# Kernel tuning notes

Measured on AMD Instinct MI355X. Metric: run time of the kernel, lower is better.

Reference implementation:

```python
import jax, jax.numpy as jnp
import numpy as np

KERNEL_SIZE = 13
SIGMA_MIN, SIGMA_MAX = 0.4, 10.0
BETA, THRESHOLD = 0.95, 1.0


@jax.custom_vjp
def spike(x):
    # Heaviside forward, snntorch ATan surrogate backward (alpha=2)
    return (x > 0).astype(x.dtype)

def _spike_fwd(x):
    return spike(x), x

def _spike_bwd(x, g):
    return (g / (1.0 + (jnp.pi * x) ** 2),)

spike.defvjp(_spike_fwd, _spike_bwd)


def setup_inputs() -> dict:
    key = jax.random.key(0)
    k1, k2 = jax.random.split(key)
    B, C, T = 32, 224, 2048
    inp = jax.random.normal(k1, (B, 1, C, T), dtype=jnp.float32)
    linear_w = jax.random.normal(k2, (1, C), dtype=jnp.float32) * (1.0 / np.sqrt(C))
    return {"inp": inp, "linear_w": linear_w}


def _forward(inp, linear_w):
    x = inp[:, 0]  # [B, C, T]
    B, C, T = x.shape
    sigma_mean = 0.5 * (SIGMA_MIN + SIGMA_MAX)
    # adaptive sigma per (batch, time): Linear over channel axis, no bias
    w = sigma_mean + jnp.einsum('bct,c->bt', x, linear_w[0]) * (SIGMA_MAX - SIGMA_MIN)
    w = jnp.clip(w, SIGMA_MIN, SIGMA_MAX)  # [B, T]

    half = KERNEL_SIZE // 2
    r = jnp.linspace(-half, half, KERNEL_SIZE)
    r_all = jnp.linspace(-half * 10, half * 10, KERNEL_SIZE * 10)
    sig = w[..., None]  # [B, T, 1]
    kern = jnp.exp(-0.5 * (r / sig) ** 2)                       # [B, T, K]
    norm = jnp.exp(-0.5 * (r_all / sig) ** 2).sum(-1, keepdims=True)
    kern = kern / norm                                          # normalized over fine grid

    # adaptive gaussian smoothing along the CHANNEL axis (per timestep kernel)
    xt = jnp.transpose(x, (0, 2, 1))                            # [B, T, C]
    padded = jnp.pad(xt, ((0, 0), (0, 0), (half, half)))        # zero pad channels
    x_mean = sum(padded[:, :, k:k + C] * kern[:, :, k:k + 1]
                 for k in range(KERNEL_SIZE))                   # [B, T, C]
    x_mean = jnp.transpose(x_mean, (0, 2, 1))                   # [B, C, T]

    I = x - jax.nn.relu(x - x_mean)                             # soft min(x, x_mean)

    # Leaky-integrate-and-fire over time (snntorch Leaky, reset-by-subtract)
    def step(mem, I_t):
        reset = jax.lax.stop_gradient((mem > THRESHOLD).astype(I_t.dtype))
        mem = BETA * mem + I_t - reset * THRESHOLD
        spk = spike(mem - THRESHOLD)
        return mem, spk

    I_seq = jnp.transpose(I, (2, 0, 1))                         # [T, B, C]
    _, spk = jax.lax.scan(step, jnp.zeros((B, C), I.dtype), I_seq)
    spk = jnp.transpose(spk, (1, 2, 0))                         # [B, C, T]
    return spk[:, None]                                         # [B, 1, C, T]


def reference(inp, linear_w):
    return _forward(inp, linear_w)
```

## Files before the change

kernel.cpp:

```cpp
#include <hip/hip_runtime.h>
#include <math.h>

#define BB 32
#define CCH 224
#define TTT 2048
#define TPB 64
#define NT  (TTT/TPB)
#define CG  28
#define NCG (CCH/CG)
#define ROWS 40
#define XROW 68
#define IROW 29

__global__ __launch_bounds__(256) void kw(
    const float* __restrict__ x, const float* __restrict__ lw,
    double* __restrict__ kernG)
{
    __shared__ double sp[4][64];
    const int b  = blockIdx.y;
    const int tl = threadIdx.x & 63;
    const int q  = threadIdx.x >> 6;
    const int t  = blockIdx.x * 64 + tl;

    const float* xb  = x + (((size_t)(b * CCH + 56 * q)) << 11) + t;
    const float* lwq = lw + 56 * q;

    double p = 0.0;
    #pragma unroll 8
    for (int i = 0; i < 56; ++i)
        p += (double)xb[(size_t)i << 11] * (double)lwq[i];
    sp[q][tl] = p;
    __syncthreads();

    if (threadIdx.x < 64) {
        double acc = (sp[0][tl] + sp[1][tl]) + (sp[2][tl] + sp[3][tl]);

        double w = 5.2 + acc * 9.6;
        w = fmin(fmax(w, 0.4), 10.0);
        double iw2 = 1.0 / (w * w);

        const double s = 120.0 / 129.0;
        double G  = exp(-0.125 * s * s * iw2);
        double G2 = G * G, G4 = G2 * G2, G8 = G4 * G4;
        double term = G, cmul = G8, norm = G;
        for (int u = 1; u <= 64; ++u) { term *= cmul; cmul *= G8; norm += term; }
        norm *= 2.0;

        double P = exp(-0.5 * iw2), P2 = P * P;
        double a = 1.0, bm = P, inv = 1.0 / norm;
        double* kr = kernG + (size_t)(b * TTT + t) * 7;
        kr[0] = inv;
        #pragma unroll
        for (int d = 1; d <= 6; ++d) {
            a *= bm; bm *= P2;
            kr[d] = a * inv;
        }
    }
}

__global__ __launch_bounds__(320) void kf(
    const float* __restrict__ x, const double* __restrict__ kernG,
    float* __restrict__ out)
{
    __shared__ __align__(16) float xs[2][ROWS][XROW];
    __shared__ double kd[2][TPB][7];
    __shared__ double Is[2][TPB][IROW];
    __shared__ unsigned long long bitsb[2][CG];

    const int b   = blockIdx.y;
    const int cgi = blockIdx.x;
    const int c0  = cgi * CG;
    const int tid = threadIdx.x;
    const int ctid = tid - 64;

    const float*  xbase = x + (((size_t)(b * CCH)) << 11);
    const double* kbase = kernG + (size_t)(b * TTT) * 7;
    float* obase = out + (((size_t)(b * CCH + c0)) << 11);

    double mem = 0.0;
    bool   r   = false;

    if (tid >= 64) {
        #pragma unroll
        for (int i2 = 0; i2 < 3; ++i2) {
            int e = ctid + i2 * 256;
            if (e < ROWS * 16) {
                int rr = e >> 4, q = e & 15;
                int cr = c0 - 6 + rr;
                float4 v = make_float4(0.f, 0.f, 0.f, 0.f);
                if (cr >= 0 && cr < CCH)
                    v = *(const float4*)(xbase + ((size_t)cr << 11) + 4 * q);
                *(float4*)&xs[0][rr][4 * q] = v;
            }
        }
        if (ctid < TPB) {
            const double* kp = kbase + (size_t)ctid * 7;
            #pragma unroll
            for (int i2 = 0; i2 < 7; ++i2) kd[0][ctid][i2] = kp[i2];
        }
    }
    __syncthreads();

    for (int k = 0; k <= NT + 1; ++k) {
        if (tid >= 64) {
            const int buf = k & 1, nbuf = (k + 1) & 1;
            float4 rv[3]; double kv[7];
            const bool st = (k + 1 <= NT - 1);
            if (st) {
                const int gt0 = (k + 1) * TPB;
                #pragma unroll
                for (int i2 = 0; i2 < 3; ++i2) {
                    int e = ctid + i2 * 256;
                    if (e < ROWS * 16) {
                        int rr = e >> 4, q = e & 15;
                        int cr = c0 - 6 + rr;
                        rv[i2] = make_float4(0.f, 0.f, 0.f, 0.f);
                        if (cr >= 0 && cr < CCH)
                            rv[i2] = *(const float4*)(xbase + ((size_t)cr << 11) + gt0 + 4 * q);
                    }
                }
                if (ctid < TPB) {
                    const double* kp = kbase + (size_t)(gt0 + ctid) * 7;
                    #pragma unroll
                    for (int i2 = 0; i2 < 7; ++i2) kv[i2] = kp[i2];
                }
            }
            if (k <= NT - 1) {
                const int t  = ctid & 63;
                const int ch = ctid >> 6;
                const int cb = 7 * ch;
                double kk7[7];
                #pragma unroll
                for (int i2 = 0; i2 < 7; ++i2) kk7[i2] = kd[buf][t][i2];
                float xv[13];
                #pragma unroll
                for (int i2 = 0; i2 < 13; ++i2) xv[i2] = xs[buf][cb + i2][t];
                #pragma unroll
                for (int c = 0; c < 7; ++c) {
                    double acc = 0.0;
                    #pragma unroll
                    for (int kk2 = 0; kk2 < 13; ++kk2) {
                        int d = kk2 < 6 ? 6 - kk2 : kk2 - 6;
                        acc = fma((double)xv[(c + kk2) % 13], kk7[d], acc);
                    }
                    double xvv = (double)xv[(c + 6) % 13];
                    double dd  = xvv - acc;
                    Is[buf][t][cb + c] = xvv - (dd > 0.0 ? dd : 0.0);
                    if (c < 6) xv[c % 13] = xs[buf][cb + c + 13][t];
                }
            }
            if (k >= 2) {
                const int j = k - 2, jb = j & 1;
                const int t0o = j * TPB;
                #pragma unroll
                for (int i2 = 0; i2 < 2; ++i2) {
                    int e = ctid + i2 * 256;
                    if (e < CG * 16) {
                        int c = e >> 4, q = e & 15;
                        unsigned long long bits = bitsb[jb][c] >> (4 * q);
                        float4 v;
                        v.x = (bits & 1ull) ? 1.0f : 0.0f;
                        v.y = (bits & 2ull) ? 1.0f : 0.0f;
                        v.z = (bits & 4ull) ? 1.0f : 0.0f;
                        v.w = (bits & 8ull) ? 1.0f : 0.0f;
                        *(float4*)(obase + ((size_t)c << 11) + t0o + 4 * q) = v;
                    }
                }
            }
            if (st) {
                #pragma unroll
                for (int i2 = 0; i2 < 3; ++i2) {
                    int e = ctid + i2 * 256;
                    if (e < ROWS * 16) {
                        int rr = e >> 4, q = e & 15;
                        *(float4*)&xs[nbuf][rr][4 * q] = rv[i2];
                    }
                }
                if (ctid < TPB) {
                    #pragma unroll
                    for (int i2 = 0; i2 < 7; ++i2) kd[nbuf][ctid][i2] = kv[i2];
                }
            }
        } else {
            if (k >= 1 && k <= NT) {
                const int p = (k - 1) & 1;
                const int c = tid;
                if (c < CG) {
                    unsigned long long bits = 0ull;
                    double va[8], vb[8];
                    #pragma unroll
                    for (int j2 = 0; j2 < 8; ++j2) va[j2] = Is[p][j2][c];
                    #pragma unroll
                    for (int g = 0; g < 64; g += 16) {
                        #pragma unroll
                        for (int j2 = 0; j2 < 8; ++j2) vb[j2] = Is[p][g + 8 + j2][c];
                        #pragma unroll
                        for (int j2 = 0; j2 < 8; ++j2) {
                            double a2 = va[j2];
                            double cm = a2 - 1.0;
                            double m1 = fma(0.95, mem, a2);
                            double m2 = fma(0.95, mem, cm);
                            mem = r ? m2 : m1;
                            r = mem > 1.0;
                            bits |= (unsigned long long)(r ? 1 : 0) << (g + j2);
                        }
                        if (g + 16 < 64) {
                            #pragma unroll
                            for (int j2 = 0; j2 < 8; ++j2) va[j2] = Is[p][g + 16 + j2][c];
                        }
                        #pragma unroll
                        for (int j2 = 0; j2 < 8; ++j2) {
                            double a2 = vb[j2];
                            double cm = a2 - 1.0;
                            double m1 = fma(0.95, mem, a2);
                            double m2 = fma(0.95, mem, cm);
                            mem = r ? m2 : m1;
                            r = mem > 1.0;
                            bits |= (unsigned long long)(r ? 1 : 0) << (g + 8 + j2);
                        }
                    }
                    bitsb[p][c] = bits;
                }
            }
        }
        __syncthreads();
    }
}

extern "C" void kernel_launch(void* const* d_in, const int* in_sizes, int n_in,
                              void* d_out, int out_size, void* d_ws, size_t ws_size,
                              hipStream_t stream)
{
    const float* x  = (const float*)d_in[0];
    const float* lw = (const float*)d_in[1];
    float* out = (float*)d_out;

    double* kernG = (double*)d_ws;

    kw<<<dim3(TTT / 64, BB), 256, 0, stream>>>(x, lw, kernG);
    kf<<<dim3(NCG, BB), 320, 0, stream>>>(x, kernG, out);
}
```

Baseline: 152.1 us.

## Deepen prefetch to two tiles ahead, raise scan wave priority, use LDS-only barrier

Global loads for the x and kernel-weight tiles are now issued two iterations ahead and held in registers across the barrier, with the LDS store of the previous prefetch done at the start of each iteration. This hides global-memory latency behind a full iteration of compute. The serial LIF scan wave gets raised instruction priority via s_setprio, since it sits on the critical path. __syncthreads is replaced by a barrier that waits only on lgkmcnt, so outstanding global loads do not stall the barrier. The cost is more live registers across iterations, and correctness now depends on global loads not being needed before the barrier.

```diff
diff --git a/kernel.cpp b/kernel.cpp
--- a/kernel.cpp
+++ b/kernel.cpp
@@ -12,6 +12,12 @@
 #define XROW 68
 #define IROW 29
 
+__device__ __forceinline__ void bar_lds() {
+    asm volatile("s_waitcnt lgkmcnt(0)" ::: "memory");
+    __builtin_amdgcn_s_barrier();
+    asm volatile("" ::: "memory");
+}
+
 __global__ __launch_bounds__(256) void kw(
     const float* __restrict__ x, const float* __restrict__ lw,
     double* __restrict__ kernG)
@@ -79,6 +85,8 @@
 
     double mem = 0.0;
     bool   r   = false;
+
+    float4 rv[3]; double kv[7];
 
     if (tid >= 64) {
         #pragma unroll
@@ -98,16 +106,47 @@
             #pragma unroll
             for (int i2 = 0; i2 < 7; ++i2) kd[0][ctid][i2] = kp[i2];
         }
+        {
+            const int gt0 = TPB;
+            #pragma unroll
+            for (int i2 = 0; i2 < 3; ++i2) {
+                int e = ctid + i2 * 256;
+                if (e < ROWS * 16) {
+                    int rr = e >> 4, q = e & 15;
+                    int cr = c0 - 6 + rr;
+                    rv[i2] = make_float4(0.f, 0.f, 0.f, 0.f);
+                    if (cr >= 0 && cr < CCH)
+                        rv[i2] = *(const float4*)(xbase + ((size_t)cr << 11) + gt0 + 4 * q);
+                }
+            }
+            if (ctid < TPB) {
+                const double* kp = kbase + (size_t)(gt0 + ctid) * 7;
+                #pragma unroll
+                for (int i2 = 0; i2 < 7; ++i2) kv[i2] = kp[i2];
+            }
+        }
     }
-    __syncthreads();
+    bar_lds();
 
     for (int k = 0; k <= NT + 1; ++k) {
         if (tid >= 64) {
             const int buf = k & 1, nbuf = (k + 1) & 1;
-            float4 rv[3]; double kv[7];
-            const bool st = (k + 1 <= NT - 1);
-            if (st) {
-                const int gt0 = (k + 1) * TPB;
+            if (k + 1 <= NT - 1) {
+                #pragma unroll
+                for (int i2 = 0; i2 < 3; ++i2) {
+                    int e = ctid + i2 * 256;
+                    if (e < ROWS * 16) {
+                        int rr = e >> 4, q = e & 15;
+                        *(float4*)&xs[nbuf][rr][4 * q] = rv[i2];
+                    }
+                }
+                if (ctid < TPB) {
+                    #pragma unroll
+                    for (int i2 = 0; i2 < 7; ++i2) kd[nbuf][ctid][i2] = kv[i2];
+                }
+            }
+            if (k + 2 <= NT - 1) {
+                const int gt0 = (k + 2) * TPB;
                 #pragma unroll
                 for (int i2 = 0; i2 < 3; ++i2) {
                     int e = ctid + i2 * 256;
@@ -123,30 +162,6 @@
                     const double* kp = kbase + (size_t)(gt0 + ctid) * 7;
                     #pragma unroll
                     for (int i2 = 0; i2 < 7; ++i2) kv[i2] = kp[i2];
-                }
-            }
-            if (k <= NT - 1) {
-                const int t  = ctid & 63;
-                const int ch = ctid >> 6;
-                const int cb = 7 * ch;
-                double kk7[7];
-                #pragma unroll
-                for (int i2 = 0; i2 < 7; ++i2) kk7[i2] = kd[buf][t][i2];
-                float xv[13];
-                #pragma unroll
-                for (int i2 = 0; i2 < 13; ++i2) xv[i2] = xs[buf][cb + i2][t];
-                #pragma unroll
-                for (int c = 0; c < 7; ++c) {
-                    double acc = 0.0;
-                    #pragma unroll
-                    for (int kk2 = 0; kk2 < 13; ++kk2) {
-                        int d = kk2 < 6 ? 6 - kk2 : kk2 - 6;
-                        acc = fma((double)xv[(c + kk2) % 13], kk7[d], acc);
-                    }
-                    double xvv = (double)xv[(c + 6) % 13];
-                    double dd  = xvv - acc;
-                    Is[buf][t][cb + c] = xvv - (dd > 0.0 ? dd : 0.0);
-                    if (c < 6) xv[c % 13] = xs[buf][cb + c + 13][t];
                 }
             }
             if (k >= 2) {
@@ -167,24 +182,35 @@
                     }
                 }
             }
-            if (st) {
-                #pragma unroll
-                for (int i2 = 0; i2 < 3; ++i2) {
-                    int e = ctid + i2 * 256;
-                    if (e < ROWS * 16) {
-                        int rr = e >> 4, q = e & 15;
-                        *(float4*)&xs[nbuf][rr][4 * q] = rv[i2];
-                    }
-                }
-                if (ctid < TPB) {
-                    #pragma unroll
-                    for (int i2 = 0; i2 < 7; ++i2) kd[nbuf][ctid][i2] = kv[i2];
+            if (k <= NT - 1) {
+                const int t  = ctid & 63;
+                const int ch = ctid >> 6;
+                const int cb = 7 * ch;
+                double kk7[7];
+                #pragma unroll
+                for (int i2 = 0; i2 < 7; ++i2) kk7[i2] = kd[buf][t][i2];
+                float xv[13];
+                #pragma unroll
+                for (int i2 = 0; i2 < 13; ++i2) xv[i2] = xs[buf][cb + i2][t];
+                #pragma unroll
+                for (int c = 0; c < 7; ++c) {
+                    double acc = 0.0;
+                    #pragma unroll
+                    for (int kk2 = 0; kk2 < 13; ++kk2) {
+                        int d = kk2 < 6 ? 6 - kk2 : kk2 - 6;
+                        acc = fma((double)xv[(c + kk2) % 13], kk7[d], acc);
+                    }
+                    double xvv = (double)xv[(c + 6) % 13];
+                    double dd  = xvv - acc;
+                    Is[buf][t][cb + c] = xvv - (dd > 0.0 ? dd : 0.0);
+                    if (c < 6) xv[c % 13] = xs[buf][cb + c + 13][t];
                 }
             }
         } else {
             if (k >= 1 && k <= NT) {
                 const int p = (k - 1) & 1;
                 const int c = tid;
+                __builtin_amdgcn_s_setprio(1);
                 if (c < CG) {
                     unsigned long long bits = 0ull;
                     double va[8], vb[8];
@@ -221,9 +247,10 @@
                     }
                     bitsb[p][c] = bits;
                 }
-            }
-        }
-        __syncthreads();
+                __builtin_amdgcn_s_setprio(0);
+            }
+        }
+        bar_lds();
     }
 }
 
```

Result: faster. 146.4 us (-3.7%).
